# Performance work log

Measured on AMD Instinct MI355X. Metric: run time of the kernel, lower is better.

The kernel has to match this reference:

```python
import jax, jax.numpy as jnp
import numpy as np

N, E, H, L, OUT, PDIM, NREL = 50000, 400000, 512, 4, 250, 2, 3
SLOPE = 0.2  # LeakyReLU negative slope


def leaky(x):
    return jnp.where(x > 0, x, SLOPE * x)


def seg_mean(msg, idx, n):
    # scatter-mean of per-edge messages onto destination nodes
    s = jax.ops.segment_sum(msg, idx, num_segments=n)
    c = jax.ops.segment_sum(jnp.ones((idx.shape[0], 1), msg.dtype), idx, num_segments=n)
    return s / jnp.maximum(c, 1.0)


def setup_inputs() -> dict:
    key = jax.random.key(0)
    ks = jax.random.split(key, 18)
    w = lambda k, shape: jax.random.normal(k, shape, dtype=jnp.float32) * 0.05
    return {
        "x_window": jax.random.normal(ks[0], (N, H), dtype=jnp.float32),
        "x_pos": jax.random.normal(ks[1], (N, PDIM), dtype=jnp.float32),
        "edge_near": jax.random.randint(ks[2], (2, E), 0, N),
        "edge_close": jax.random.randint(ks[3], (2, E), 0, N),
        "edge_sim": jax.random.randint(ks[4], (2, E), 0, N),
        "W_pre": w(ks[5], (H, H)),            # pretransform_win (no bias)
        "W_post": w(ks[6], (H, H)),           # post_plot_transform linear (no bias)
        "Wl": w(ks[7], (L, NREL, H, H)),      # SAGE neighbor transform per layer/relation
        "Wr": w(ks[8], (L, NREL, H, H)),      # SAGE self transform per layer/relation
        "Wpos": w(ks[9], (L, NREL, PDIM, H)), # edge_embed: relative-position embedding
        "Wg": w(ks[10], (L, H, H)),           # global vector injection per layer
        "seed": w(ks[11], (L, H)),            # GMPool_I seed query per layer
        "Wk": w(ks[12], (L, H, H)),
        "Wv": w(ks[13], (L, H, H)),
        "W_out": w(ks[14], (H, OUT)),
        "b_out": jnp.zeros((OUT,), jnp.float32),
    }


def reference(x_window, x_pos, edge_near, edge_close, edge_sim,
              W_pre, W_post, Wl, Wr, Wpos, Wg, seed, Wk, Wv, W_out, b_out):
    edges = (edge_near, edge_close, edge_sim)
    # pretransform + post_plot_transform: LeakyReLU -> Linear -> LeakyReLU
    x = leaky(leaky(x_window @ W_pre) @ W_post)
    inv_sqrt = np.float32(1.0 / np.sqrt(H))
    for l in range(L):
        # GMPool_I attention pooling over all nodes -> one global vector [H]
        attn = jax.nn.softmax(((x @ Wk[l]) @ seed[l]) * inv_sqrt)  # [N]
        g = attn @ (x @ Wv[l])                                      # [H]
        gterm = g @ Wg[l]                                           # [H]
        acc = jnp.zeros_like(x)
        for r in range(NREL):
            src, dst = edges[r][0], edges[r][1]
            # message = neighbor feature + relative-position edge embedding
            msg = x[src] + (x_pos[src] - x_pos[dst]) @ Wpos[l, r]   # [E,H]
            agg = seg_mean(msg, dst, N)                             # [N,H]
            acc = acc + agg @ Wl[l, r] + x @ Wr[l, r] + gterm
        x = leaky(acc / np.float32(NREL))  # HeteroConv aggr='mean' + LeakyReLU
    return x @ W_out + b_out
```

## Files before the change

kernel.cpp:

```cpp
#include <hip/hip_runtime.h>

#define NN 50000
#define EE 400000
#define HH 512
#define LL 4
#define OUTC 250
#define MP 50048
#define HH2 (HH*HH)
#define NPW 512
#define NBLK 49
#define INV_SQRT_H 0.044194173824159216f

typedef unsigned short u16;
typedef unsigned char u8;
typedef __attribute__((ext_vector_type(8))) unsigned short u16x8;
typedef __attribute__((ext_vector_type(8))) short s16x8;
typedef __attribute__((ext_vector_type(4))) float f32x4;
typedef __attribute__((ext_vector_type(2))) float f32x2;

__device__ __forceinline__ float b2f(u16 v) {
  union { unsigned u; float f; } c; c.u = ((unsigned)v) << 16; return c.f;
}
__device__ __forceinline__ u16 f2b(float f) {
  union { float f; unsigned u; } c; c.f = f;
  unsigned r = c.u + 0x7fffu + ((c.u >> 16) & 1u);
  return (u16)(r >> 16);
}
__device__ __forceinline__ float leakyf(float v) { return v > 0.f ? v : 0.2f * v; }

__device__ __forceinline__ void async16(const void* g, void* l) {
  __builtin_amdgcn_global_load_lds((const __attribute__((address_space(1))) void*)g,
                                   (__attribute__((address_space(3))) void*)l,
                                   16, 0, 0);
}

__global__ void k_hist(const int* __restrict__ e0, const int* __restrict__ e1,
                       const int* __restrict__ e2, int* __restrict__ cnt) {
  int r = blockIdx.y;
  const int* dst = (r == 0 ? e0 : r == 1 ? e1 : e2) + EE;
  int i = blockIdx.x * 256 + threadIdx.x;
  if (i < EE) atomicAdd(&cnt[r * NN + dst[i]], 1);
}

__global__ void k_scan1(const int* __restrict__ cnt, int* __restrict__ offs,
                        float* __restrict__ invc, int* __restrict__ bsum) {
  int r = blockIdx.y, b = blockIdx.x, t = threadIdx.x;
  int i = b * 1024 + t;
  int v = (i < NN) ? cnt[r * NN + i] : 0;
  __shared__ int sm[1024];
  sm[t] = v;
  __syncthreads();
#pragma unroll
  for (int d = 1; d < 1024; d <<= 1) {
    int u = (t >= d) ? sm[t - d] : 0;
    __syncthreads();
    sm[t] += u;
    __syncthreads();
  }
  if (i < NN) {
    offs[r * (NN + 1) + i] = sm[t] - v;
    invc[r * NN + i] = 1.f / (float)(v > 1 ? v : 1);
  }
  if (t == 1023) bsum[r * NBLK + b] = sm[t];
}

__global__ void k_scan2(int* __restrict__ bsum) {
  int t = threadIdx.x;
  int r = t >> 6, lane = t & 63;
  if (r >= 3) return;
  int orig = (lane < NBLK) ? bsum[r * NBLK + lane] : 0;
  int v = orig;
#pragma unroll
  for (int d = 1; d < 64; d <<= 1) {
    int u = __shfl_up(v, d);
    if (lane >= d) v += u;
  }
  if (lane < NBLK) bsum[r * NBLK + lane] = v - orig;
}

__global__ void k_scan3(const int* __restrict__ bsum, int* __restrict__ offs,
                        int* __restrict__ cursor) {
  int r = blockIdx.y, b = blockIdx.x, t = threadIdx.x;
  int i = b * 1024 + t;
  if (i < NN) {
    int v = offs[r * (NN + 1) + i] + bsum[r * NBLK + b];
    offs[r * (NN + 1) + i] = v;
    cursor[r * NN + i] = v;
  }
  if (b == 0 && t == 0) offs[r * (NN + 1) + NN] = EE;
}

__global__ void k_fill(const int* __restrict__ e0, const int* __restrict__ e1,
                       const int* __restrict__ e2,
                       int* __restrict__ cursor, int* __restrict__ csr) {
  int r = blockIdx.y;
  const int* ep = (r == 0 ? e0 : r == 1 ? e1 : e2);
  int i = blockIdx.x * 256 + threadIdx.x;
  if (i >= EE) return;
  int s = ep[i], d = ep[EE + i];
  int slot = atomicAdd(&cursor[r * NN + d], 1);
  csr[r * EE + slot] = s;
}

__global__ void k_pvec(const int* __restrict__ offs, const int* __restrict__ csr,
                       const float2* __restrict__ pos, float* __restrict__ P) {
  int r = blockIdx.y;
  int i = blockIdx.x * 256 + threadIdx.x;
  if (i >= NN) return;
  const int* o = offs + r * (NN + 1);
  const int* cs = csr + (size_t)r * EE;
  int b = o[i], e = o[i + 1];
  float sx = 0.f, sy = 0.f;
  for (int k = b; k < e; ++k) {
    float2 p = pos[cs[k]];
    sx += p.x; sy += p.y;
  }
  float2 pd = pos[i];
  float c = (float)(e - b);
  P[(size_t)r * NN * 2 + 2 * i]     = sx - c * pd.x;
  P[(size_t)r * NN * 2 + 2 * i + 1] = sy - c * pd.y;
}

__global__ void k_transT14(const float* __restrict__ Wl, const float* __restrict__ W_pre,
                           const float* __restrict__ W_post,
                           u16* __restrict__ wlT, u16* __restrict__ wpreT,
                           u16* __restrict__ wpostT) {
  __shared__ float sm[32][33];
  int z = blockIdx.z;
  const float* Wm; u16* WTm;
  if (z < 12)      { Wm = Wl + (size_t)z * HH2;  WTm = wlT + (size_t)z * HH2; }
  else if (z == 12){ Wm = W_pre;                  WTm = wpreT; }
  else             { Wm = W_post;                 WTm = wpostT; }
  int r0 = blockIdx.y * 32, c0 = blockIdx.x * 32;
  int tx = threadIdx.x, ty = threadIdx.y;
#pragma unroll
  for (int i = 0; i < 4; ++i)
    sm[ty + i * 8][tx] = Wm[(size_t)(r0 + ty + i * 8) * HH + c0 + tx];
  __syncthreads();
#pragma unroll
  for (int i = 0; i < 4; ++i)
    WTm[(size_t)(c0 + ty + i * 8) * HH + r0 + tx] = f2b(sm[tx][ty + i * 8]);
}

__global__ void k_sum3T(const float* __restrict__ Wr, u16* __restrict__ WT) {
  __shared__ float sm[32][33];
  int l = blockIdx.z;
  const float* W3 = Wr + (size_t)l * 3 * HH2;
  u16* WTm = WT + (size_t)l * HH2;
  int r0 = blockIdx.y * 32, c0 = blockIdx.x * 32;
  int tx = threadIdx.x, ty = threadIdx.y;
#pragma unroll
  for (int i = 0; i < 4; ++i) {
    size_t idx = (size_t)(r0 + ty + i * 8) * HH + c0 + tx;
    sm[ty + i * 8][tx] = W3[idx] + W3[HH2 + idx] + W3[2 * (size_t)HH2 + idx];
  }
  __syncthreads();
#pragma unroll
  for (int i = 0; i < 4; ++i)
    WTm[(size_t)(c0 + ty + i * 8) * HH + r0 + tx] = f2b(sm[tx][ty + i * 8]);
}

__global__ void k_transpose_pad(const float* __restrict__ W, u16* __restrict__ WT,
                                int rows, int cols, int tcols) {
  int idx = blockIdx.x * 256 + threadIdx.x;
  if (idx >= rows * tcols) return;
  int r = idx % rows, c = idx / rows;
  float v = (c < cols) ? W[(size_t)r * cols + c] : 0.f;
  WT[(size_t)c * rows + r] = f2b(v);
}

#define CVT_BLK ((NN * HH / 8 + 255) / 256)
__global__ void k_cvt_zero(const float* __restrict__ in, u16* __restrict__ out,
                           u16* a, u16* b, u16* c, u16* d, u16* e) {
  int blk = blockIdx.x;
  if (blk < CVT_BLK) {
    int i = blk * 256 + threadIdx.x;
    if (i >= NN * HH / 8) return;
    const float4 x = *(const float4*)(in + (size_t)i * 8);
    const float4 y = *(const float4*)(in + (size_t)i * 8 + 4);
    u16x8 o;
    o[0] = f2b(x.x); o[1] = f2b(x.y); o[2] = f2b(x.z); o[3] = f2b(x.w);
    o[4] = f2b(y.x); o[5] = f2b(y.y); o[6] = f2b(y.z); o[7] = f2b(y.w);
    *(u16x8*)(out + (size_t)i * 8) = o;
  } else {
    int i = (blk - CVT_BLK) * 256 + threadIdx.x;
    const int per = (MP - NN) * HH;
    if (i >= per * 5) return;
    int sel = i / per, rem = i - sel * per;
    u16* p = sel == 0 ? a : sel == 1 ? b : sel == 2 ? c : sel == 3 ? d : e;
    p[(size_t)NN * HH + rem] = 0;
  }
}

__global__ void k_kvec(const float* __restrict__ Wk, const float* __restrict__ seed,
                       float* __restrict__ kvec) {
  int l = blockIdx.x;
  const float* Wkl = Wk + (size_t)l * HH2;
  const float* sdl = seed + (size_t)l * HH;
  float* kv = kvec + (size_t)l * HH;
  int w = threadIdx.x >> 6, lane = threadIdx.x & 63;
  float sv[8];
#pragma unroll
  for (int i = 0; i < 8; ++i) sv[i] = sdl[lane * 8 + i];
  for (int row = w; row < HH; row += 8) {
    const float* p = Wkl + (size_t)row * HH + lane * 8;
    float d = 0.f;
#pragma unroll
    for (int i = 0; i < 8; ++i) d += p[i] * sv[i];
#pragma unroll
    for (int o = 32; o > 0; o >>= 1) d += __shfl_xor(d, o);
    if (lane == 0) kv[row] = d;
  }
}

__global__ void k_pool2g(const float* __restrict__ part, const float* __restrict__ Wv,
                         const float* __restrict__ Wg, float* __restrict__ gterm) {
  __shared__ float red[512];
  __shared__ float gv[HH];
  __shared__ float g[HH];
  int t = threadIdx.x;
  red[t] = part[(size_t)t * 514];
  __syncthreads();
  for (int s = 256; s > 0; s >>= 1) {
    if (t < s) red[t] = fmaxf(red[t], red[t + s]);
    __syncthreads();
  }
  float M = red[0];
  float s = 0.f, z = 0.f;
  for (int w = 0; w < NPW; ++w) {
    const float* p = part + (size_t)w * 514;
    float e = __expf(p[0] - M);
    z += e * p[1];
    s += e * p[2 + t];
  }
  gv[t] = s / z;
  __syncthreads();
  float a = 0.f;
  for (int i = 0; i < HH; ++i) a += gv[i] * Wv[(size_t)i * HH + t];
  g[t] = a;
  __syncthreads();
  float b = 0.f;
  for (int i = 0; i < HH; ++i) b += g[i] * Wg[(size_t)i * HH + t];
  gterm[t] = b;
}

__device__ __forceinline__ void acc_fp8x8(float* acc, uint2 v) {
  f32x2 a0 = __builtin_amdgcn_cvt_pk_f32_fp8(v.x, false);
  f32x2 a1 = __builtin_amdgcn_cvt_pk_f32_fp8(v.x, true);
  f32x2 a2 = __builtin_amdgcn_cvt_pk_f32_fp8(v.y, false);
  f32x2 a3 = __builtin_amdgcn_cvt_pk_f32_fp8(v.y, true);
  acc[0] += a0[0]; acc[1] += a0[1]; acc[2] += a1[0]; acc[3] += a1[1];
  acc[4] += a2[0]; acc[5] += a2[1]; acc[6] += a3[0]; acc[7] += a3[1];
}

__global__ void k_spmm_pool(const int* __restrict__ offs, const int* __restrict__ csr,
                            const float* __restrict__ invc, const float* __restrict__ P,
                            const float* __restrict__ wposL, const u16* __restrict__ x,
                            const u8* __restrict__ x8,
                            u16* __restrict__ agg, const float* __restrict__ kvec,
                            float* __restrict__ part) {
  int r = blockIdx.y;
  int lane = threadIdx.x & 63;
  if (r == 3) {
    if (blockIdx.x >= NPW / 4) return;
    int gw = (blockIdx.x * 256 + threadIdx.x) >> 6;
    float kl[8];
#pragma unroll
    for (int i = 0; i < 8; ++i) kl[i] = kvec[lane * 8 + i];
    float m = -1e30f, Z = 0.f;
    float acc[8] = {0, 0, 0, 0, 0, 0, 0, 0};
    for (int n = gw; n < NN; n += NPW) {
      u16x8 v = *(const u16x8*)(x + (size_t)n * HH + lane * 8);
      float xl[8], d = 0.f;
#pragma unroll
      for (int i = 0; i < 8; ++i) { xl[i] = b2f(v[i]); d += xl[i] * kl[i]; }
#pragma unroll
      for (int o = 32; o > 0; o >>= 1) d += __shfl_xor(d, o);
      d *= INV_SQRT_H;
      float mn = fmaxf(m, d);
      float c = __expf(m - mn), w = __expf(d - mn);
      Z = Z * c + w;
#pragma unroll
      for (int i = 0; i < 8; ++i) acc[i] = acc[i] * c + w * xl[i];
      m = mn;
    }
    float* p = part + (size_t)gw * 514;
#pragma unroll
    for (int i = 0; i < 8; ++i) p[2 + lane * 8 + i] = acc[i];
    if (lane == 0) { p[0] = m; p[1] = Z; }
    return;
  }
  int wv = __builtin_amdgcn_readfirstlane((int)(blockIdx.x * 256 + threadIdx.x) >> 6);
  if (wv >= NN) return;
  const int* o = offs + r * (NN + 1);
  const int* cs = csr + (size_t)r * EE;
  const float* wpos = wposL + (size_t)r * 2 * HH;
  int beg = o[wv], end = o[wv + 1];
  float acc[8] = {0, 0, 0, 0, 0, 0, 0, 0};
  int k = beg;
  for (; k + 7 < end; k += 8) {
    int s[8];
#pragma unroll
    for (int j = 0; j < 8; ++j) s[j] = cs[k + j];
    uint2 v[8];
#pragma unroll
    for (int j = 0; j < 8; ++j) v[j] = *(const uint2*)(x8 + (size_t)s[j] * HH + lane * 8);
#pragma unroll
    for (int j = 0; j < 8; ++j) acc_fp8x8(acc, v[j]);
  }
  for (; k + 3 < end; k += 4) {
    int s[4];
#pragma unroll
    for (int j = 0; j < 4; ++j) s[j] = cs[k + j];
    uint2 v[4];
#pragma unroll
    for (int j = 0; j < 4; ++j) v[j] = *(const uint2*)(x8 + (size_t)s[j] * HH + lane * 8);
#pragma unroll
    for (int j = 0; j < 4; ++j) acc_fp8x8(acc, v[j]);
  }
  for (; k < end; ++k) {
    uint2 v0 = *(const uint2*)(x8 + (size_t)cs[k] * HH + lane * 8);
    acc_fp8x8(acc, v0);
  }
  float px = P[(size_t)r * NN * 2 + 2 * wv], py = P[(size_t)r * NN * 2 + 2 * wv + 1];
  float ic = invc[(size_t)r * NN + wv];
  u16x8 out;
#pragma unroll
  for (int i = 0; i < 8; ++i) {
    float w0 = wpos[lane * 8 + i];
    float w1 = wpos[HH + lane * 8 + i];
    float v = (acc[i] + px * w0 + py * w1) * ic;
    out[i] = f2b(v);
  }
  __builtin_nontemporal_store(out, (u16x8*)(agg + ((size_t)r * MP + wv) * HH + lane * 8));
}

__global__ __launch_bounds__(256) void k_gemm(
    const u16* __restrict__ A0, const u16* __restrict__ A1,
    const u16* __restrict__ A2, const u16* __restrict__ A3,
    const u16* __restrict__ B0, const u16* __restrict__ B1,
    const u16* __restrict__ B2, const u16* __restrict__ B3,
    int nkt, int mode, float alpha, const float* __restrict__ gvec,
    u16* __restrict__ outB, u8* __restrict__ out8, float* __restrict__ outF,
    const float* __restrict__ bias, int M, int Nout, int G, int gx)
{
  __shared__ u16 lsA[128 * 64];
  __shared__ u16 lsB[128 * 64];
  const int tid = threadIdx.x;
  const int wave = tid >> 6, lane = tid & 63;
  const int wm = (wave >> 1) * 64, wn = (wave & 1) * 64;

  const int gid = blockIdx.x;
  const int q = G >> 3, rr = G & 7;
  const int xk = gid & 7, idx = gid >> 3;
  const int tl = xk * q + (xk < rr ? xk : rr) + idx;
  const int rowM0 = (tl / gx) * 128, colN0 = (tl % gx) * 128;

  f32x4 acc[4][4];
#pragma unroll
  for (int i = 0; i < 4; ++i)
#pragma unroll
    for (int j = 0; j < 4; ++j) acc[i][j] = (f32x4){0.f, 0.f, 0.f, 0.f};

  const int rowT = wave * 8 + (lane >> 3);
  const int c8 = lane & 7;
  int aoff[2][4], boff[2][4];
#pragma unroll
  for (int K0 = 0; K0 < 2; ++K0)
#pragma unroll
    for (int f = 0; f < 4; ++f) {
      const int cb = K0 * 4 + (lane >> 4);
      const int mm = wm + f * 16 + (lane & 15);
      const int nn = wn + f * 16 + (lane & 15);
      aoff[K0][f] = mm * 64 + ((cb ^ (mm & 7)) << 3);
      boff[K0][f] = nn * 64 + ((cb ^ (nn & 7)) << 3);
    }

  const int nkb = nkt >> 3;
  for (int kb = 0; kb < nkb; ++kb) {
    const u16* As = kb == 0 ? A0 : (kb == 1 ? A1 : (kb == 2 ? A2 : A3));
    const u16* Bs = kb == 0 ? B0 : (kb == 1 ? B1 : (kb == 2 ? B2 : B3));
    for (int k8 = 0; k8 < 8; ++k8) {
      const int koff = k8 * 64;
#pragma unroll
      for (int i = 0; i < 4; ++i) {
        const int r = i * 32 + rowT;
        const int scol = (c8 ^ (r & 7)) * 8;
        async16(As + (size_t)(rowM0 + r) * HH + koff + scol, &lsA[i * 2048 + wave * 512]);
        async16(Bs + (size_t)(colN0 + r) * HH + koff + scol, &lsB[i * 2048 + wave * 512]);
      }
      __syncthreads();
#pragma unroll
      for (int K0 = 0; K0 < 2; ++K0) {
        s16x8 af[4], bfr[4];
#pragma unroll
        for (int f = 0; f < 4; ++f) {
          af[f] = *(const s16x8*)&lsA[aoff[K0][f]];
          bfr[f] = *(const s16x8*)&lsB[boff[K0][f]];
        }
#pragma unroll
        for (int fm = 0; fm < 4; ++fm)
#pragma unroll
          for (int fn = 0; fn < 4; ++fn)
            acc[fm][fn] = __builtin_amdgcn_mfma_f32_16x16x32_bf16(af[fm], bfr[fn], acc[fm][fn], 0, 0, 0);
      }
      __syncthreads();
    }
  }

#pragma unroll
  for (int fm = 0; fm < 4; ++fm) {
#pragma unroll
    for (int fn = 0; fn < 4; ++fn) {
#pragma unroll
      for (int r = 0; r < 4; ++r) {
        const int row = rowM0 + wm + fm * 16 + ((lane >> 4) << 2) + r;
        const int col = colN0 + wn + fn * 16 + (lane & 15);
        float v = acc[fm][fn][r];
        if (mode == 0) {
          v = leakyf(v * alpha + (gvec ? gvec[col] : 0.f));
          __builtin_nontemporal_store(f2b(v), &outB[(size_t)row * HH + col]);
          if (out8) {
            int pk = __builtin_amdgcn_cvt_pk_fp8_f32(v, v, 0, false);
            __builtin_nontemporal_store((u8)pk, &out8[(size_t)row * HH + col]);
          }
        } else {
          if (row < M && col < Nout)
            __builtin_nontemporal_store(v + (bias ? bias[col] : 0.f), &outF[(size_t)row * Nout + col]);
        }
      }
    }
  }
}

extern "C" void kernel_launch(void* const* d_in, const int* in_sizes, int n_in,
                              void* d_out, int out_size, void* d_ws, size_t ws_size,
                              hipStream_t stream) {
  (void)in_sizes; (void)n_in; (void)out_size;
  const float* x_window = (const float*)d_in[0];
  const float* x_pos    = (const float*)d_in[1];
  const int*   e0 = (const int*)d_in[2];
  const int*   e1 = (const int*)d_in[3];
  const int*   e2 = (const int*)d_in[4];
  const float* W_pre  = (const float*)d_in[5];
  const float* W_post = (const float*)d_in[6];
  const float* Wl   = (const float*)d_in[7];
  const float* Wr   = (const float*)d_in[8];
  const float* Wpos = (const float*)d_in[9];
  const float* Wg   = (const float*)d_in[10];
  const float* seed = (const float*)d_in[11];
  const float* Wk   = (const float*)d_in[12];
  const float* Wv   = (const float*)d_in[13];
  const float* W_out= (const float*)d_in[14];
  const float* b_out= (const float*)d_in[15];
  float* out = (float*)d_out;

  char* base = (char*)d_ws;
  size_t off = 0;
  auto alloc = [&](size_t bytes) -> char* {
    char* p = base + off;
    off += (bytes + 255) & ~(size_t)255;
    return p;
  };
  u16* x_a   = (u16*)alloc((size_t)MP * HH * 2);
  u16* x_b   = (u16*)alloc((size_t)MP * HH * 2);
  u16* agg0  = (u16*)alloc((size_t)MP * HH * 2);
  u16* agg1  = (u16*)alloc((size_t)MP * HH * 2);
  u16* agg2  = (u16*)alloc((size_t)MP * HH * 2);
  u8*  x8    = (u8*)alloc((size_t)MP * HH);
  u16* wlT   = (u16*)alloc((size_t)12 * HH2 * 2);
  u16* wrsT  = (u16*)alloc((size_t)4 * HH2 * 2);
  u16* wpreT = (u16*)alloc((size_t)HH2 * 2);
  u16* wpostT= (u16*)alloc((size_t)HH2 * 2);
  u16* woutT = (u16*)alloc((size_t)256 * HH * 2);
  int* offs  = (int*)alloc((size_t)3 * (NN + 1) * 4);
  int* curs  = (int*)alloc((size_t)3 * NN * 4);
  int* cnt   = (int*)alloc((size_t)3 * NN * 4);
  int* csr   = (int*)alloc((size_t)3 * EE * 4);
  float* invc = (float*)alloc((size_t)3 * NN * 4);
  float* P    = (float*)alloc((size_t)3 * NN * 2 * 4);
  float* kvec  = (float*)alloc((size_t)LL * HH * 4);
  float* gterm = (float*)alloc(HH * 4);
  int* bsum  = (int*)alloc((size_t)3 * NBLK * 4);
  float* part  = (float*)curs;
  if (off > ws_size) return;

  hipMemsetAsync(cnt, 0, (size_t)3 * NN * 4, stream);

  k_hist<<<dim3((EE + 255) / 256, 3), 256, 0, stream>>>(e0, e1, e2, cnt);
  k_scan1<<<dim3(NBLK, 3), 1024, 0, stream>>>(cnt, offs, invc, bsum);
  k_scan2<<<1, 256, 0, stream>>>(bsum);
  k_scan3<<<dim3(NBLK, 3), 1024, 0, stream>>>(bsum, offs, curs);
  k_fill<<<dim3((EE + 255) / 256, 3), 256, 0, stream>>>(e0, e1, e2, curs, csr);
  k_pvec<<<dim3((NN + 255) / 256, 3), 256, 0, stream>>>(offs, csr, (const float2*)x_pos, P);

  k_transT14<<<dim3(16, 16, 14), dim3(32, 8), 0, stream>>>(Wl, W_pre, W_post,
                                                           wlT, wpreT, wpostT);
  k_sum3T<<<dim3(16, 16, 4), dim3(32, 8), 0, stream>>>(Wr, wrsT);
  k_transpose_pad<<<(HH * 256) / 256, 256, 0, stream>>>(W_out, woutT, HH, OUTC, 256);
  k_kvec<<<LL, 512, 0, stream>>>(Wk, seed, kvec);

  const int padBlk = ((MP - NN) * HH * 5 + 255) / 256;
  k_cvt_zero<<<CVT_BLK + padBlk, 256, 0, stream>>>(x_window, x_b, x_a, x_b, agg0, agg1, agg2);

  const u16* nul = nullptr;
  const int G4 = 4 * (MP / 128), G2 = 2 * (MP / 128);
  k_gemm<<<G4, 256, 0, stream>>>(x_b, nul, nul, nul, wpreT, nul, nul, nul,
                                 8, 0, 1.f, nullptr, agg0, nullptr, nullptr, nullptr, NN, HH, G4, 4);
  k_gemm<<<G4, 256, 0, stream>>>(agg0, nul, nul, nul, wpostT, nul, nul, nul,
                                 8, 0, 1.f, nullptr, x_a, x8, nullptr, nullptr, NN, HH, G4, 4);

  u16* cur = x_a; u16* nxt = x_b;
  for (int l = 0; l < LL; ++l) {
    k_spmm_pool<<<dim3(NN / 4, 4), 256, 0, stream>>>(offs, csr, invc, P,
                                                     Wpos + (size_t)l * 3 * 2 * HH, cur, x8, agg0,
                                                     kvec + (size_t)l * HH, part);
    k_pool2g<<<1, 512, 0, stream>>>(part, Wv + (size_t)l * HH2, Wg + (size_t)l * HH2, gterm);
    k_gemm<<<G4, 256, 0, stream>>>(
        agg0, agg1, agg2, cur,
        wlT + (size_t)(l * 3 + 0) * HH2, wlT + (size_t)(l * 3 + 1) * HH2,
        wlT + (size_t)(l * 3 + 2) * HH2, wrsT + (size_t)l * HH2,
        32, 0, (1.f / 3.f), gterm, nxt, (l < LL - 1) ? x8 : nullptr, nullptr, nullptr, NN, HH, G4, 4);
    u16* t = cur; cur = nxt; nxt = t;
  }
  k_gemm<<<G2, 256, 0, stream>>>(cur, nul, nul, nul, woutT, nul, nul, nul,
                                 8, 1, 1.f, nullptr, nullptr, nullptr, out, b_out, NN, OUTC, G2, 2);
}
```

Before: 2.317 ms.

## Fuse pool finalize into spmm via last-block atomic and stage fp8 stores

```diff
diff --git a/kernel.cpp b/kernel.cpp
--- a/kernel.cpp
+++ b/kernel.cpp
@@ -8,6 +8,7 @@
 #define MP 50048
 #define HH2 (HH*HH)
 #define NPW 512
+#define NPB (NPW/4)
 #define NBLK 49
 #define INV_SQRT_H 0.044194173824159216f
 
@@ -213,37 +214,6 @@
   }
 }
 
-__global__ void k_pool2g(const float* __restrict__ part, const float* __restrict__ Wv,
-                         const float* __restrict__ Wg, float* __restrict__ gterm) {
-  __shared__ float red[512];
-  __shared__ float gv[HH];
-  __shared__ float g[HH];
-  int t = threadIdx.x;
-  red[t] = part[(size_t)t * 514];
-  __syncthreads();
-  for (int s = 256; s > 0; s >>= 1) {
-    if (t < s) red[t] = fmaxf(red[t], red[t + s]);
-    __syncthreads();
-  }
-  float M = red[0];
-  float s = 0.f, z = 0.f;
-  for (int w = 0; w < NPW; ++w) {
-    const float* p = part + (size_t)w * 514;
-    float e = __expf(p[0] - M);
-    z += e * p[1];
-    s += e * p[2 + t];
-  }
-  gv[t] = s / z;
-  __syncthreads();
-  float a = 0.f;
-  for (int i = 0; i < HH; ++i) a += gv[i] * Wv[(size_t)i * HH + t];
-  g[t] = a;
-  __syncthreads();
-  float b = 0.f;
-  for (int i = 0; i < HH; ++i) b += g[i] * Wg[(size_t)i * HH + t];
-  gterm[t] = b;
-}
-
 __device__ __forceinline__ void acc_fp8x8(float* acc, uint2 v) {
   f32x2 a0 = __builtin_amdgcn_cvt_pk_f32_fp8(v.x, false);
   f32x2 a1 = __builtin_amdgcn_cvt_pk_f32_fp8(v.x, true);
@@ -258,11 +228,17 @@
                             const float* __restrict__ wposL, const u16* __restrict__ x,
                             const u8* __restrict__ x8,
                             u16* __restrict__ agg, const float* __restrict__ kvec,
-                            float* __restrict__ part) {
+                            float* __restrict__ part, int* __restrict__ poolcnt,
+                            const float* __restrict__ Wv, const float* __restrict__ Wg,
+                            float* __restrict__ gterm) {
+  __shared__ float sred[256];
+  __shared__ float sgv[HH];
+  __shared__ float sg[HH];
+  __shared__ int slast;
   int r = blockIdx.y;
   int lane = threadIdx.x & 63;
   if (r == 3) {
-    if (blockIdx.x >= NPW / 4) return;
+    if (blockIdx.x >= NPB) return;
     int gw = (blockIdx.x * 256 + threadIdx.x) >> 6;
     float kl[8];
 #pragma unroll
@@ -288,6 +264,48 @@
 #pragma unroll
     for (int i = 0; i < 8; ++i) p[2 + lane * 8 + i] = acc[i];
     if (lane == 0) { p[0] = m; p[1] = Z; }
+    __threadfence();
+    __syncthreads();
+    if (threadIdx.x == 0) slast = (atomicAdd(poolcnt, 1) == NPB - 1) ? 1 : 0;
+    __syncthreads();
+    if (!slast) return;
+    if (threadIdx.x == 0) atomicExch(poolcnt, 0);
+    __threadfence();
+    int t = threadIdx.x;
+    volatile const float* vp = part;
+    sred[t] = fmaxf(vp[(size_t)t * 514], vp[(size_t)(t + 256) * 514]);
+    __syncthreads();
+    for (int s = 128; s > 0; s >>= 1) {
+      if (t < s) sred[t] = fmaxf(sred[t], sred[t + s]);
+      __syncthreads();
+    }
+    float M = sred[0];
+    float s0 = 0.f, s1 = 0.f, z = 0.f;
+    for (int w = 0; w < NPW; ++w) {
+      volatile const float* p2 = part + (size_t)w * 514;
+      float e = __expf(p2[0] - M);
+      z += e * p2[1];
+      s0 += e * p2[2 + t];
+      s1 += e * p2[2 + t + 256];
+    }
+    float invz = 1.f / z;
+    sgv[t] = s0 * invz; sgv[t + 256] = s1 * invz;
+    __syncthreads();
+    float a0 = 0.f, a1 = 0.f;
+    for (int i = 0; i < HH; ++i) {
+      float gvi = sgv[i];
+      a0 += gvi * Wv[(size_t)i * HH + t];
+      a1 += gvi * Wv[(size_t)i * HH + t + 256];
+    }
+    sg[t] = a0; sg[t + 256] = a1;
+    __syncthreads();
+    float b0 = 0.f, b1 = 0.f;
+    for (int i = 0; i < HH; ++i) {
+      float gi = sg[i];
+      b0 += gi * Wg[(size_t)i * HH + t];
+      b1 += gi * Wg[(size_t)i * HH + t + 256];
+    }
+    gterm[t] = b0; gterm[t + 256] = b1;
     return;
   }
   int wv = __builtin_amdgcn_readfirstlane((int)(blockIdx.x * 256 + threadIdx.x) >> 6);
@@ -408,28 +426,38 @@
     }
   }
 
+  u8* l8 = (u8*)lsA;
 #pragma unroll
   for (int fm = 0; fm < 4; ++fm) {
 #pragma unroll
     for (int fn = 0; fn < 4; ++fn) {
 #pragma unroll
       for (int r = 0; r < 4; ++r) {
-        const int row = rowM0 + wm + fm * 16 + ((lane >> 4) << 2) + r;
-        const int col = colN0 + wn + fn * 16 + (lane & 15);
+        const int rit = wm + fm * 16 + ((lane >> 4) << 2) + r;
+        const int cit = wn + fn * 16 + (lane & 15);
+        const int row = rowM0 + rit, col = colN0 + cit;
         float v = acc[fm][fn][r];
         if (mode == 0) {
           v = leakyf(v * alpha + (gvec ? gvec[col] : 0.f));
-          __builtin_nontemporal_store(f2b(v), &outB[(size_t)row * HH + col]);
+          outB[(size_t)row * HH + col] = f2b(v);
           if (out8) {
             int pk = __builtin_amdgcn_cvt_pk_fp8_f32(v, v, 0, false);
-            __builtin_nontemporal_store((u8)pk, &out8[(size_t)row * HH + col]);
+            l8[rit * 128 + cit] = (u8)pk;
           }
         } else {
           if (row < M && col < Nout)
-            __builtin_nontemporal_store(v + (bias ? bias[col] : 0.f), &outF[(size_t)row * Nout + col]);
+            outF[(size_t)row * Nout + col] = v + (bias ? bias[col] : 0.f);
         }
       }
     }
+  }
+  if (mode == 0 && out8) {
+    __syncthreads();
+    const int rit = tid >> 1, hoff = (tid & 1) * 64;
+    const uint4* src = (const uint4*)(l8 + rit * 128 + hoff);
+    uint4 v0 = src[0], v1 = src[1], v2 = src[2], v3 = src[3];
+    uint4* dst = (uint4*)(out8 + (size_t)(rowM0 + rit) * HH + colN0 + hoff);
+    dst[0] = v0; dst[1] = v1; dst[2] = v2; dst[3] = v3;
   }
 }
 
@@ -482,10 +510,12 @@
   float* kvec  = (float*)alloc((size_t)LL * HH * 4);
   float* gterm = (float*)alloc(HH * 4);
   int* bsum  = (int*)alloc((size_t)3 * NBLK * 4);
+  int* poolcnt = (int*)alloc(256);
   float* part  = (float*)curs;
   if (off > ws_size) return;
 
   hipMemsetAsync(cnt, 0, (size_t)3 * NN * 4, stream);
+  hipMemsetAsync(poolcnt, 0, 256, stream);
 
   k_hist<<<dim3((EE + 255) / 256, 3), 256, 0, stream>>>(e0, e1, e2, cnt);
   k_scan1<<<dim3(NBLK, 3), 1024, 0, stream>>>(cnt, offs, invc, bsum);
@@ -514,8 +544,9 @@
   for (int l = 0; l < LL; ++l) {
     k_spmm_pool<<<dim3(NN / 4, 4), 256, 0, stream>>>(offs, csr, invc, P,
                                                      Wpos + (size_t)l * 3 * 2 * HH, cur, x8, agg0,
-                                                     kvec + (size_t)l * HH, part);
-    k_pool2g<<<1, 512, 0, stream>>>(part, Wv + (size_t)l * HH2, Wg + (size_t)l * HH2, gterm);
+                                                     kvec + (size_t)l * HH, part, poolcnt,
+                                                     Wv + (size_t)l * HH2, Wg + (size_t)l * HH2,
+                                                     gterm);
     k_gemm<<<G4, 256, 0, stream>>>(
         agg0, agg1, agg2, cur,
         wlT + (size_t)(l * 3 + 0) * HH2, wlT + (size_t)(l * 3 + 1) * HH2,
```

Measured after the change: 3.552 ms. 53.3% more time.
